# Optimization experiments

Hardware: AMD Instinct MI355X
Metric: run time of the kernel (lower is better)

The kernel has to match this reference:

```python
import jax, jax.numpy as jnp
from jax import lax
import numpy as np

B, L, D = 4, 4096, 1024
H = 16
HD = D // H          # 64
WIN = 256
NC = L // WIN
N_ITER = 50          # entmax-bisect iterations (entmax library default)
LN_EPS = 1e-5


def _p(x, am1):
    # clamp(x, min=0) ** (1/(alpha-1))
    return jnp.clip(x, 0.0) ** (1.0 / am1)


def entmax_bisect(X, alpha):
    """alpha-entmax along the last axis via bisection. alpha broadcastable to X."""
    am1 = alpha - 1.0
    Xs = X * am1
    d = X.shape[-1]
    max_val = Xs.max(axis=-1, keepdims=True)
    tau_lo = max_val - 1.0                       # 1 ** (alpha-1)
    tau_hi = max_val - (1.0 / d) ** am1
    f_lo = _p(Xs - tau_lo, am1).sum(-1, keepdims=True) - 1.0
    dm0 = tau_hi - tau_lo

    def body(i, carry):
        tau_lo, dm, _ = carry
        dm = dm * 0.5
        tau_m = tau_lo + dm
        f_m = _p(Xs - tau_m, am1).sum(-1, keepdims=True) - 1.0
        tau_lo = jnp.where(f_m * f_lo >= 0, tau_m, tau_lo)
        return (tau_lo, dm, tau_m)

    tau_lo, dm, tau_m = lax.fori_loop(0, N_ITER, body, (tau_lo, dm0, tau_lo))
    p = _p(Xs - tau_m, am1)
    return p / p.sum(-1, keepdims=True)          # ensure_sum_one


def setup_inputs() -> dict:
    key = jax.random.key(0)
    ks = jax.random.split(key, 4)
    x = jax.random.normal(ks[0], (B, L, D), jnp.float32)
    alpha = jnp.full((H,), 1.5, jnp.float32)
    qkv_w = 0.02 * jax.random.normal(ks[1], (3 * D, D), jnp.float32)
    qkv_b = jnp.zeros((3 * D,), jnp.float32)
    o_w = 0.02 * jax.random.normal(ks[2], (D, D), jnp.float32)
    o_b = jnp.zeros((D,), jnp.float32)
    ln_gamma = jnp.ones((D,), jnp.float32)
    ln_beta = jnp.zeros((D,), jnp.float32)
    return {"x": x, "alpha": alpha, "qkv_w": qkv_w, "qkv_b": qkv_b,
            "o_w": o_w, "o_b": o_b, "ln_gamma": ln_gamma, "ln_beta": ln_beta}


def reference(x, alpha, qkv_w, qkv_b, o_w, o_b, ln_gamma, ln_beta):
    # qkv projection -> [B, H, L, 3*HD]
    qkv = (x @ qkv_w.T + qkv_b).reshape(B, L, H, 3 * HD).transpose(0, 2, 1, 3)
    q, k, v = jnp.split(qkv, 3, axis=-1)
    # block-diagonal windows (span=None => k/v chunks coincide with q chunks)
    qc = q.reshape(B, H, NC, WIN, HD)
    kc = k.reshape(B, H, NC, WIN, HD)
    vc = v.reshape(B, H, NC, WIN, HD)
    scores = jnp.einsum('bhcqd,bhckd->bhcqk', qc, kc) / np.sqrt(HD).astype(np.float32)
    weights = entmax_bisect(scores, alpha.reshape(1, H, 1, 1, 1))
    out = jnp.einsum('bhcqk,bhckd->bhcqd', weights, vc)
    out = out.reshape(B, H, L, HD).transpose(0, 2, 1, 3).reshape(B, L, D)
    # layer norm
    mu = out.mean(-1, keepdims=True)
    var = out.var(-1, keepdims=True)
    out = (out - mu) * lax.rsqrt(var + LN_EPS) * ln_gamma + ln_beta
    return out @ o_w.T + o_b
```

## Files before the change

kernel.cpp:

```cpp
#include <hip/hip_runtime.h>

typedef unsigned short u16;
typedef unsigned int   u32;
typedef __attribute__((ext_vector_type(8))) short bf16x8;
typedef __attribute__((ext_vector_type(4))) float f32x4;
typedef __attribute__((ext_vector_type(8))) u16  u16x8;

__device__ __forceinline__ float b2f(u16 u) {
    union { u32 i; float f; } v; v.i = ((u32)u) << 16; return v.f;
}
__device__ __forceinline__ u16 f2b(float f) {
    u32 i = __float_as_uint(f);
    u32 r = (i + 0x7FFFu + ((i >> 16) & 1u)) >> 16;
    return (u16)r;
}
__device__ __forceinline__ bool is_bf16(const u32* gprobe) { return *gprobe == 0x3F803F80u; }

__device__ __forceinline__ void load_lds16(const void* g, void* l) {
    __builtin_amdgcn_global_load_lds((__attribute__((address_space(1))) void*)g,
                                     (__attribute__((address_space(3))) void*)l, 16, 0, 0);
}

__global__ __launch_bounds__(256) void cvt_kern(const void* __restrict__ src, u16* __restrict__ dst,
                                                int n8, const u32* __restrict__ gprobe) {
    const bool isb = is_bf16(gprobe);
    const int i = blockIdx.x * 256 + threadIdx.x;
    if (i >= n8) return;
    if (isb) {
        ((u16x8*)dst)[i] = ((const u16x8*)src)[i];
    } else {
        const float* s = (const float*)src + (size_t)i * 8;
        u16x8 o;
        #pragma unroll
        for (int j = 0; j < 8; j++) o[j] = f2b(s[j]);
        ((u16x8*)dst)[i] = o;
    }
}

__global__ __launch_bounds__(256) void gemm_bt(const u16* __restrict__ A, const u16* __restrict__ B,
                                               const void* __restrict__ bias,
                                               u16* __restrict__ Cb, float* __restrict__ Cf,
                                               const u32* __restrict__ gprobe, int out_mode,
                                               int M, int N, int K) {
    __shared__ u16 lsA[128 * 32];
    __shared__ u16 lsB[128 * 32];
    const int tid  = threadIdx.x;
    const int wave = tid >> 6, lane = tid & 63;
    const int m0 = blockIdx.y * 128, n0 = blockIdx.x * 128;
    const int wr = wave >> 1, wc = wave & 1;

    f32x4 acc[4][4] = {};

    const int srow = wave * 16 + (lane >> 2);
    const int scol = (lane & 3) * 8;
    const u16* gA0 = A + (size_t)(m0 + srow) * K + scol;
    const u16* gB0 = B + (size_t)(n0 + srow) * K + scol;
    u16* lA0 = &lsA[wave * 512];
    u16* lB0 = &lsB[wave * 512];
    const size_t rstep = (size_t)64 * K;

    for (int k0 = 0; k0 < K; k0 += 32) {
        __syncthreads();
        load_lds16(gA0 + k0,         lA0);
        load_lds16(gA0 + k0 + rstep, lA0 + 2048);
        load_lds16(gB0 + k0,         lB0);
        load_lds16(gB0 + k0 + rstep, lB0 + 2048);
        __syncthreads();

        bf16x8 af[4], bfr[4];
        #pragma unroll
        for (int mi = 0; mi < 4; mi++)
            af[mi] = *(const bf16x8*)&lsA[(wr * 64 + mi * 16 + (lane & 15)) * 32 + (lane >> 4) * 8];
        #pragma unroll
        for (int ni = 0; ni < 4; ni++)
            bfr[ni] = *(const bf16x8*)&lsB[(wc * 64 + ni * 16 + (lane & 15)) * 32 + (lane >> 4) * 8];
        #pragma unroll
        for (int mi = 0; mi < 4; mi++)
            #pragma unroll
            for (int ni = 0; ni < 4; ni++)
                acc[mi][ni] = __builtin_amdgcn_mfma_f32_16x16x32_bf16(af[mi], bfr[ni], acc[mi][ni], 0, 0, 0);
    }

    const bool isb     = is_bf16(gprobe);
    const bool store_b = (out_mode == 0) || isb;
    const int g = lane >> 4, cc = lane & 15;
    #pragma unroll
    for (int ni = 0; ni < 4; ni++) {
        const int col = n0 + wc * 64 + ni * 16 + cc;
        const float bv = isb ? b2f(((const u16*)bias)[col]) : ((const float*)bias)[col];
        #pragma unroll
        for (int mi = 0; mi < 4; mi++) {
            const int row = m0 + wr * 64 + mi * 16 + g * 4;
            #pragma unroll
            for (int i = 0; i < 4; i++) {
                const float v = acc[mi][ni][i] + bv;
                const size_t idx = (size_t)(row + i) * N + col;
                if (store_b) Cb[idx] = f2b(v);
                else         Cf[idx] = v;
            }
        }
    }
}

__device__ __forceinline__ void bfly_sum4(float (&a)[4]) {
    #pragma unroll
    for (int m = 1; m <= 8; m <<= 1)
        #pragma unroll
        for (int i = 0; i < 4; i++) a[i] += __shfl_xor(a[i], m, 64);
}

__device__ __forceinline__ void entmax2_rows(f32x4 (&s)[16]) {
    float mx[4] = {-3e38f, -3e38f, -3e38f, -3e38f};
    #pragma unroll
    for (int nt = 0; nt < 16; nt++)
        #pragma unroll
        for (int i = 0; i < 4; i++) mx[i] = fmaxf(mx[i], s[nt][i]);
    #pragma unroll
    for (int m = 1; m <= 8; m <<= 1)
        #pragma unroll
        for (int i = 0; i < 4; i++) mx[i] = fmaxf(mx[i], __shfl_xor(mx[i], m, 64));

    float tau[4];
    #pragma unroll
    for (int i = 0; i < 4; i++) tau[i] = mx[i] - 1.0f;

    #pragma unroll 1
    for (int it = 0; it < 10; it++) {
        float a2[4] = {0.f, 0.f, 0.f, 0.f};
        float a1[4] = {0.f, 0.f, 0.f, 0.f};
        #pragma unroll
        for (int nt = 0; nt < 16; nt++)
            #pragma unroll
            for (int i = 0; i < 4; i++) {
                float t = fmaxf(s[nt][i] - tau[i], 0.0f);
                a2[i] = fmaf(t, t, a2[i]);
                a1[i] += t;
            }
        bfly_sum4(a2);
        bfly_sum4(a1);
        #pragma unroll
        for (int i = 0; i < 4; i++)
            tau[i] += (a2[i] - 1.0f) * 0.5f * __builtin_amdgcn_rcpf(a1[i]);
    }

    float ss[4] = {0.f, 0.f, 0.f, 0.f};
    #pragma unroll
    for (int nt = 0; nt < 16; nt++)
        #pragma unroll
        for (int i = 0; i < 4; i++) {
            float t = fmaxf(s[nt][i] - tau[i], 0.0f);
            float p = t * t;
            s[nt][i] = p;
            ss[i] += p;
        }
    bfly_sum4(ss);
    float inv[4];
    #pragma unroll
    for (int i = 0; i < 4; i++) inv[i] = 1.0f / ss[i];
    #pragma unroll
    for (int nt = 0; nt < 16; nt++)
        #pragma unroll
        for (int i = 0; i < 4; i++) s[nt][i] *= inv[i];
}

__device__ __forceinline__ void entmax_gen_rows(f32x4 (&s)[16], float e, float dm0) {
    float mx[4] = {-3e38f, -3e38f, -3e38f, -3e38f};
    #pragma unroll
    for (int nt = 0; nt < 16; nt++)
        #pragma unroll
        for (int i = 0; i < 4; i++) mx[i] = fmaxf(mx[i], s[nt][i]);
    #pragma unroll
    for (int m = 1; m <= 8; m <<= 1)
        #pragma unroll
        for (int i = 0; i < 4; i++) mx[i] = fmaxf(mx[i], __shfl_xor(mx[i], m, 64));

    float tau_lo[4], tau_m[4], f_lo[4];
    #pragma unroll
    for (int i = 0; i < 4; i++) { tau_lo[i] = mx[i] - 1.0f; tau_m[i] = tau_lo[i]; }
    {
        float a[4] = {0.f, 0.f, 0.f, 0.f};
        #pragma unroll
        for (int nt = 0; nt < 16; nt++)
            #pragma unroll
            for (int i = 0; i < 4; i++) {
                float t = fmaxf(s[nt][i] - tau_lo[i], 0.0f);
                a[i] += (t > 0.0f) ? __expf(e * __logf(t)) : 0.0f;
            }
        bfly_sum4(a);
        #pragma unroll
        for (int i = 0; i < 4; i++) f_lo[i] = a[i] - 1.0f;
    }
    float dm = dm0;
    #pragma unroll 1
    for (int it = 0; it < 26; it++) {
        dm *= 0.5f;
        #pragma unroll
        for (int i = 0; i < 4; i++) tau_m[i] = tau_lo[i] + dm;
        float a[4] = {0.f, 0.f, 0.f, 0.f};
        #pragma unroll
        for (int nt = 0; nt < 16; nt++)
            #pragma unroll
            for (int i = 0; i < 4; i++) {
                float t = fmaxf(s[nt][i] - tau_m[i], 0.0f);
                a[i] += (t > 0.0f) ? __expf(e * __logf(t)) : 0.0f;
            }
        bfly_sum4(a);
        #pragma unroll
        for (int i = 0; i < 4; i++)
            tau_lo[i] = ((a[i] - 1.0f) * f_lo[i] >= 0.0f) ? tau_m[i] : tau_lo[i];
    }
    float ss[4] = {0.f, 0.f, 0.f, 0.f};
    #pragma unroll
    for (int nt = 0; nt < 16; nt++)
        #pragma unroll
        for (int i = 0; i < 4; i++) {
            float t = fmaxf(s[nt][i] - tau_m[i], 0.0f);
            float p = (t > 0.0f) ? __expf(e * __logf(t)) : 0.0f;
            s[nt][i] = p;
            ss[i] += p;
        }
    bfly_sum4(ss);
    float inv[4];
    #pragma unroll
    for (int i = 0; i < 4; i++) inv[i] = 1.0f / ss[i];
    #pragma unroll
    for (int nt = 0; nt < 16; nt++)
        #pragma unroll
        for (int i = 0; i < 4; i++) s[nt][i] *= inv[i];
}

__global__ __launch_bounds__(256, 2) void attn_win(const u16* __restrict__ qkv,
                                                   const void* __restrict__ alpha, u16* __restrict__ att,
                                                   const u32* __restrict__ gprobe) {
    __shared__ u16 Vt[64 * 264];
    __shared__ u16 Kl[256 * 72];
    __shared__ u16 Wl[4 * 16 * 72];
    const int tid  = threadIdx.x;
    const int wave = tid >> 6, lane = tid & 63;
    const int c = blockIdx.x, h = blockIdx.y, b = blockIdx.z;
    const int g = lane >> 4, cc = lane & 15;

    const float av  = is_bf16(gprobe) ? b2f(((const u16*)alpha)[h]) : ((const float*)alpha)[h];
    const float am1 = av - 1.0f;
    const float e   = 1.0f / am1;
    const bool  sq  = (e == 2.0f);
    const float scl = am1 * 0.125f;
    const float dm0 = 1.0f - exp2f(-8.0f * am1);

    const size_t tok0 = (size_t)b * 4096 + (size_t)c * 256;
    const u16* qbase = qkv + tok0 * 3072 + h * 192;
    const u16* kbase = qbase + 64;
    const u16* vbase = qbase + 128;
    u16* wl = &Wl[wave * (16 * 72)];

    {
        const int kr = tid >> 3, kc2 = tid & 7;
        #pragma unroll
        for (int it = 0; it < 8; it++) {
            const int row = it * 32 + kr;
            bf16x8 kv = *(const bf16x8*)(kbase + (size_t)row * 3072 + kc2 * 8);
            *(bf16x8*)&Kl[row * 72 + kc2 * 8] = kv;
        }
    }

    {
        const int d = tid & 63, tg = tid >> 6;
        #pragma unroll
        for (int j = 0; j < 8; j++) {
            const int t0 = tg * 64 + j * 8;
            u16x8 tmp;
            #pragma unroll
            for (int i = 0; i < 8; i++)
                tmp[i] = vbase[(size_t)(t0 + i) * 3072 + d];
            *(u16x8*)&Vt[d * 264 + t0] = tmp;
        }
    }
    __syncthreads();

    bf16x8 q0, q1;
    {
        const u16* qr = qbase + (size_t)(wave * 16 + cc) * 3072 + g * 8;
        q0 = *(const bf16x8*)qr;
        q1 = *(const bf16x8*)(qr + 32);
    }

    for (int ch = 0; ch < 4; ch++) {
        const int r0 = ch * 64 + wave * 16;

        bf16x8 n0, n1;
        {
            const int chn = (ch + 1) & 3;
            const u16* qr = qbase + (size_t)(chn * 64 + wave * 16 + cc) * 3072 + g * 8;
            n0 = *(const bf16x8*)qr;
            n1 = *(const bf16x8*)(qr + 32);
        }

        f32x4 s[16] = {};
        #pragma unroll
        for (int nt = 0; nt < 16; nt++) {
            const u16* krow = &Kl[(nt * 16 + cc) * 72 + g * 8];
            bf16x8 bk0 = *(const bf16x8*)krow;
            bf16x8 bk1 = *(const bf16x8*)(krow + 32);
            s[nt] = __builtin_amdgcn_mfma_f32_16x16x32_bf16(q0, bk0, s[nt], 0, 0, 0);
            s[nt] = __builtin_amdgcn_mfma_f32_16x16x32_bf16(q1, bk1, s[nt], 0, 0, 0);
        }
        #pragma unroll
        for (int nt = 0; nt < 16; nt++)
            #pragma unroll
            for (int i = 0; i < 4; i++) s[nt][i] *= scl;

        if (sq) entmax2_rows(s);
        else    entmax_gen_rows(s, e, dm0);

        f32x4 o[4] = {};
        #pragma unroll
        for (int kc = 0; kc < 8; kc++) {
            #pragma unroll
            for (int t = 0; t < 2; t++) {
                const int nt = kc * 2 + t;
                #pragma unroll
                for (int i = 0; i < 4; i++)
                    wl[(g * 4 + i) * 40 + t * 16 + cc] = f2b(s[nt][i]);
            }
            bf16x8 aw = *(const bf16x8*)&wl[cc * 40 + g * 8];
            #pragma unroll
            for (int nd = 0; nd < 4; nd++) {
                bf16x8 bv = *(const bf16x8*)&Vt[(nd * 16 + cc) * 264 + kc * 32 + g * 8];
                o[nd] = __builtin_amdgcn_mfma_f32_16x16x32_bf16(aw, bv, o[nd], 0, 0, 0);
            }
        }

        #pragma unroll
        for (int nd = 0; nd < 4; nd++)
            #pragma unroll
            for (int i = 0; i < 4; i++)
                wl[(g * 4 + i) * 72 + nd * 16 + cc] = f2b(o[nd][i]);
        #pragma unroll
        for (int p = 0; p < 2; p++) {
            const int row = p * 8 + (lane >> 3);
            u16x8 val = *(const u16x8*)&wl[row * 72 + (lane & 7) * 8];
            *(u16x8*)(att + (size_t)(tok0 + r0 + row) * 1024 + h * 64 + (lane & 7) * 8) = val;
        }

        q0 = n0; q1 = n1;
    }
}

__global__ __launch_bounds__(256) void ln_kern(const u16* __restrict__ att, const void* __restrict__ gam,
                                               const void* __restrict__ bet, u16* __restrict__ out,
                                               const u32* __restrict__ gprobe) {
    const bool isb = is_bf16(gprobe);
    const int tid = threadIdx.x;
    const int wave = tid >> 6, lane = tid & 63;
    const size_t tok = (size_t)blockIdx.x * 4 + wave;
    const u16* p = att + tok * 1024 + lane * 16;
    u16x8 v0 = *(const u16x8*)p;
    u16x8 v1 = *(const u16x8*)(p + 8);
    float x[16];
    #pragma unroll
    for (int j = 0; j < 8; j++) { x[j] = b2f(v0[j]); x[j + 8] = b2f(v1[j]); }
    float s = 0.f, s2 = 0.f;
    #pragma unroll
    for (int j = 0; j < 16; j++) { s += x[j]; s2 = fmaf(x[j], x[j], s2); }
    #pragma unroll
    for (int m = 1; m <= 32; m <<= 1) { s += __shfl_xor(s, m, 64); s2 += __shfl_xor(s2, m, 64); }
    const float mean = s * (1.0f / 1024.0f);
    const float var  = s2 * (1.0f / 1024.0f) - mean * mean;
    const float rs   = rsqrtf(var + 1e-5f);

    float gv[16], bv[16];
    if (isb) {
        const u16* gp = (const u16*)gam + lane * 16;
        const u16* bp = (const u16*)bet + lane * 16;
        u16x8 g0 = *(const u16x8*)gp, g1 = *(const u16x8*)(gp + 8);
        u16x8 b0 = *(const u16x8*)bp, b1 = *(const u16x8*)(bp + 8);
        #pragma unroll
        for (int j = 0; j < 8; j++) {
            gv[j] = b2f(g0[j]); gv[j + 8] = b2f(g1[j]);
            bv[j] = b2f(b0[j]); bv[j + 8] = b2f(b1[j]);
        }
    } else {
        const float* gp = (const float*)gam + lane * 16;
        const float* bp = (const float*)bet + lane * 16;
        #pragma unroll
        for (int j = 0; j < 16; j++) { gv[j] = gp[j]; bv[j] = bp[j]; }
    }

    u16x8 w0, w1;
    #pragma unroll
    for (int j = 0; j < 8; j++) {
        w0[j] = f2b((x[j]     - mean) * rs * gv[j]     + bv[j]);
        w1[j] = f2b((x[j + 8] - mean) * rs * gv[j + 8] + bv[j + 8]);
    }
    u16* op = out + tok * 1024 + lane * 16;
    *(u16x8*)op       = w0;
    *(u16x8*)(op + 8) = w1;
}

extern "C" void kernel_launch(void* const* d_in, const int* in_sizes, int n_in,
                              void* d_out, int out_size, void* d_ws, size_t ws_size,
                              hipStream_t stream) {
    const void* x      = d_in[0];
    const void* alpha  = d_in[1];
    const void* qkv_w  = d_in[2];
    const void* qkv_b  = d_in[3];
    const void* o_w    = d_in[4];
    const void* o_b    = d_in[5];
    const u32*  gprobe = (const u32*)d_in[6];
    const void* gam    = d_in[6];
    const void* bet    = d_in[7];

    u16* xb  = (u16*)d_ws;
    u16* wq  = xb + (size_t)16384 * 1024;
    u16* wo  = wq + (size_t)3072 * 1024;
    u16* qkv = wo + (size_t)1024 * 1024;
    u16* att = (u16*)d_out;
    u16* ln  = xb;

    dim3 blk(256);
    cvt_kern<<<dim3((16384 * 1024 / 8 + 255) / 256), blk, 0, stream>>>(x, xb, 16384 * 1024 / 8, gprobe);
    cvt_kern<<<dim3((3072 * 1024 / 8 + 255) / 256), blk, 0, stream>>>(qkv_w, wq, 3072 * 1024 / 8, gprobe);
    cvt_kern<<<dim3((1024 * 1024 / 8 + 255) / 256), blk, 0, stream>>>(o_w, wo, 1024 * 1024 / 8, gprobe);
    gemm_bt<<<dim3(3072 / 128, 16384 / 128), blk, 0, stream>>>(xb, wq, qkv_b, qkv, nullptr, gprobe, 0,
                                                               16384, 3072, 1024);
    attn_win<<<dim3(16, 16, 4), blk, 0, stream>>>(qkv, alpha, att, gprobe);
    ln_kern<<<dim3(4096), blk, 0, stream>>>(att, gam, bet, ln, gprobe);
    gemm_bt<<<dim3(1024 / 128, 16384 / 128), blk, 0, stream>>>(ln, wo, o_b, (u16*)d_out, (float*)d_out,
                                                               gprobe, 1, 16384, 1024, 1024);
}
```

Before: 536.8 us.

## Use 512-thread attention blocks with XOR-swizzled unpadded LDS tiles

The windowed attention kernel grows from 4 to 8 waves per block, so each wave handles 2 row chunks instead of 4, and it asks for 4 blocks per CU instead of 2 to raise occupancy during the entmax bisection. The padded K, V-transpose and weight-staging LDS arrays are replaced by unpadded ones using an XOR swizzle on byte offsets to avoid bank conflicts. The register prefetch of the next Q chunk is dropped. The tighter launch bounds cap registers per thread and may cause spills of the 64-float score array.

```diff
diff --git a/kernel.cpp b/kernel.cpp
--- a/kernel.cpp
+++ b/kernel.cpp
@@ -229,12 +229,12 @@
         for (int i = 0; i < 4; i++) s[nt][i] *= inv[i];
 }
 
-__global__ __launch_bounds__(256, 2) void attn_win(const u16* __restrict__ qkv,
+__global__ __launch_bounds__(512, 4) void attn_win(const u16* __restrict__ qkv,
                                                    const void* __restrict__ alpha, u16* __restrict__ att,
                                                    const u32* __restrict__ gprobe) {
-    __shared__ u16 Vt[64 * 264];
-    __shared__ u16 Kl[256 * 72];
-    __shared__ u16 Wl[4 * 16 * 72];
+    __shared__ u16 Kl[256 * 64];
+    __shared__ u16 Vt[64 * 256];
+    __shared__ u16 Wl[8 * 16 * 64];
     const int tid  = threadIdx.x;
     const int wave = tid >> 6, lane = tid & 63;
     const int c = blockIdx.x, h = blockIdx.y, b = blockIdx.z;
@@ -251,56 +251,50 @@
     const u16* qbase = qkv + tok0 * 3072 + h * 192;
     const u16* kbase = qbase + 64;
     const u16* vbase = qbase + 128;
-    u16* wl = &Wl[wave * (16 * 72)];
+    char* wl = (char*)&Wl[wave * (16 * 64)];
 
     {
         const int kr = tid >> 3, kc2 = tid & 7;
         #pragma unroll
-        for (int it = 0; it < 8; it++) {
-            const int row = it * 32 + kr;
+        for (int it = 0; it < 4; it++) {
+            const int row = it * 64 + kr;
             bf16x8 kv = *(const bf16x8*)(kbase + (size_t)row * 3072 + kc2 * 8);
-            *(bf16x8*)&Kl[row * 72 + kc2 * 8] = kv;
+            const int off = (row * 128 + kc2 * 16) ^ ((row & 7) << 4);
+            *(bf16x8*)((char*)Kl + off) = kv;
         }
     }
 
     {
         const int d = tid & 63, tg = tid >> 6;
         #pragma unroll
-        for (int j = 0; j < 8; j++) {
-            const int t0 = tg * 64 + j * 8;
+        for (int j = 0; j < 4; j++) {
+            const int t0 = tg * 32 + j * 8;
             u16x8 tmp;
             #pragma unroll
             for (int i = 0; i < 8; i++)
                 tmp[i] = vbase[(size_t)(t0 + i) * 3072 + d];
-            *(u16x8*)&Vt[d * 264 + t0] = tmp;
+            const int off = (d * 512 + t0 * 2) ^ ((d & 7) << 4);
+            *(u16x8*)((char*)Vt + off) = tmp;
         }
     }
     __syncthreads();
 
-    bf16x8 q0, q1;
-    {
-        const u16* qr = qbase + (size_t)(wave * 16 + cc) * 3072 + g * 8;
-        q0 = *(const bf16x8*)qr;
-        q1 = *(const bf16x8*)(qr + 32);
-    }
-
-    for (int ch = 0; ch < 4; ch++) {
-        const int r0 = ch * 64 + wave * 16;
-
-        bf16x8 n0, n1;
-        {
-            const int chn = (ch + 1) & 3;
-            const u16* qr = qbase + (size_t)(chn * 64 + wave * 16 + cc) * 3072 + g * 8;
-            n0 = *(const bf16x8*)qr;
-            n1 = *(const bf16x8*)(qr + 32);
-        }
+    for (int ch = 0; ch < 2; ch++) {
+        const int r0 = ch * 128 + wave * 16;
+
+        const u16* qr = qbase + (size_t)(r0 + cc) * 3072 + g * 8;
+        bf16x8 q0 = *(const bf16x8*)qr;
+        bf16x8 q1 = *(const bf16x8*)(qr + 32);
 
         f32x4 s[16] = {};
         #pragma unroll
         for (int nt = 0; nt < 16; nt++) {
-            const u16* krow = &Kl[(nt * 16 + cc) * 72 + g * 8];
-            bf16x8 bk0 = *(const bf16x8*)krow;
-            bf16x8 bk1 = *(const bf16x8*)(krow + 32);
+            const int krow = nt * 16 + cc;
+            const int swz  = (cc & 7) << 4;
+            const int off0 = (krow * 128 + g * 16) ^ swz;
+            const int off1 = (krow * 128 + g * 16 + 64) ^ swz;
+            bf16x8 bk0 = *(const bf16x8*)((const char*)Kl + off0);
+            bf16x8 bk1 = *(const bf16x8*)((const char*)Kl + off1);
             s[nt] = __builtin_amdgcn_mfma_f32_16x16x32_bf16(q0, bk0, s[nt], 0, 0, 0);
             s[nt] = __builtin_amdgcn_mfma_f32_16x16x32_bf16(q1, bk1, s[nt], 0, 0, 0);
         }
@@ -319,13 +313,18 @@
             for (int t = 0; t < 2; t++) {
                 const int nt = kc * 2 + t;
                 #pragma unroll
-                for (int i = 0; i < 4; i++)
-                    wl[(g * 4 + i) * 40 + t * 16 + cc] = f2b(s[nt][i]);
-            }
-            bf16x8 aw = *(const bf16x8*)&wl[cc * 40 + g * 8];
+                for (int i = 0; i < 4; i++) {
+                    const int wrow = g * 4 + i;
+                    const int off  = (wrow * 128 + t * 32 + cc * 2) ^ ((wrow & 7) << 4);
+                    *(u16*)(wl + off) = f2b(s[nt][i]);
+                }
+            }
+            bf16x8 aw = *(const bf16x8*)(wl + ((cc * 128 + g * 16) ^ ((cc & 7) << 4)));
             #pragma unroll
             for (int nd = 0; nd < 4; nd++) {
-                bf16x8 bv = *(const bf16x8*)&Vt[(nd * 16 + cc) * 264 + kc * 32 + g * 8];
+                const int vrow = nd * 16 + cc;
+                const int voff = (vrow * 512 + kc * 64 + g * 16) ^ ((cc & 7) << 4);
+                bf16x8 bv = *(const bf16x8*)((const char*)Vt + voff);
                 o[nd] = __builtin_amdgcn_mfma_f32_16x16x32_bf16(aw, bv, o[nd], 0, 0, 0);
             }
         }
@@ -333,16 +332,18 @@
         #pragma unroll
         for (int nd = 0; nd < 4; nd++)
             #pragma unroll
-            for (int i = 0; i < 4; i++)
-                wl[(g * 4 + i) * 72 + nd * 16 + cc] = f2b(o[nd][i]);
+            for (int i = 0; i < 4; i++) {
+                const int wrow = g * 4 + i;
+                const int off  = (wrow * 128 + nd * 32 + cc * 2) ^ ((wrow & 7) << 4);
+                *(u16*)(wl + off) = f2b(o[nd][i]);
+            }
         #pragma unroll
         for (int p = 0; p < 2; p++) {
             const int row = p * 8 + (lane >> 3);
-            u16x8 val = *(const u16x8*)&wl[row * 72 + (lane & 7) * 8];
+            const int off = (row * 128 + (lane & 7) * 16) ^ ((row & 7) << 4);
+            u16x8 val = *(const u16x8*)(wl + off);
             *(u16x8*)(att + (size_t)(tok0 + r0 + row) * 1024 + h * 64 + (lane & 7) * 8) = val;
         }
-
-        q0 = n0; q1 = n1;
     }
 }
 
@@ -423,7 +424,7 @@
     cvt_kern<<<dim3((1024 * 1024 / 8 + 255) / 256), blk, 0, stream>>>(o_w, wo, 1024 * 1024 / 8, gprobe);
     gemm_bt<<<dim3(3072 / 128, 16384 / 128), blk, 0, stream>>>(xb, wq, qkv_b, qkv, nullptr, gprobe, 0,
                                                                16384, 3072, 1024);
-    attn_win<<<dim3(16, 16, 4), blk, 0, stream>>>(qkv, alpha, att, gprobe);
+    attn_win<<<dim3(16, 16, 4), dim3(512), 0, stream>>>(qkv, alpha, att, gprobe);
     ln_kern<<<dim3(4096), blk, 0, stream>>>(att, gam, bet, ln, gprobe);
     gemm_bt<<<dim3(1024 / 128, 16384 / 128), blk, 0, stream>>>(ln, wo, o_b, (u16*)d_out, (float*)d_out,
                                                                gprobe, 1, 16384, 1024, 1024);
```

Result: slower. 716.2 us (+33.4%).
